# Kernel tuning notes

Measured on AMD Instinct MI355X. Metric: run time of the kernel, lower is better.

## Reference

```python
import jax, jax.numpy as jnp
import numpy as np

BN_EPS = 1e-5

def setup_inputs() -> dict:
    key = jax.random.key(0)
    k1, k2, k3 = jax.random.split(key, 3)
    B, N, C, K, O = 4, 16384, 64, 16, 64
    x = jax.random.normal(k1, (B, N, C), dtype=jnp.float32)
    idx = jax.random.randint(k2, (B, N, K), 0, N, dtype=jnp.int32)
    weight = jax.random.normal(k3, (O, 2 * C), dtype=jnp.float32) * 0.05
    gamma = jnp.ones((O,), dtype=jnp.float32)
    beta = jnp.zeros((O,), dtype=jnp.float32)
    return {"x": x, "idx": idx, "weight": weight, "gamma": gamma, "beta": beta}

def reference(x, idx, weight, gamma, beta):
    # x: [B,N,C], idx: [B,N,k] kNN indices into N
    B, N, C = x.shape
    k = idx.shape[2]
    # irregular gather: neighbor features [B,N,k,C]
    batch_ix = jnp.arange(B)[:, None, None]
    neighbor = x[batch_ix, idx]                     # [B,N,k,C]
    center = x[:, :, None, :]                       # [B,N,1,C]
    diff = neighbor - center                        # [B,N,k,C]
    edge = jnp.concatenate([jnp.broadcast_to(center, (B, N, k, C)), diff], axis=-1)  # [B,N,k,2C]
    # 1x1 conv == per-edge linear transform: [B,N,k,O]
    h = jnp.einsum('bnkc,oc->bnko', edge, weight)
    # BatchNorm2d in training mode: stats over (B,N,k) per output channel
    mean = jnp.mean(h, axis=(0, 1, 2))
    var = jnp.var(h, axis=(0, 1, 2))
    h = (h - mean) * jax.lax.rsqrt(var + BN_EPS) * gamma + beta
    h = jax.nn.relu(h)
    # max-pool over k neighbors -> [B,N,O]
    out = jnp.max(h, axis=2)
    return out
```

## Files before the change

kernel.cpp:

```cpp
#include <hip/hip_runtime.h>
#include <math.h>

#define BN_EPS 1e-5f

constexpr int B_ = 4, N_ = 16384, C_ = 64, K_ = 16, O_ = 64;
constexpr int ROWS = B_ * N_;
constexpr int ROWS_PER_BLK = 64;
constexpr int NBLK_AB = ROWS / ROWS_PER_BLK;

__global__ __launch_bounds__(256) void pass_a(const float* __restrict__ x,
                                              const float* __restrict__ w,
                                              float* __restrict__ y1,
                                              float* __restrict__ y2) {
    __shared__ float w1m[64 * 65];
    __shared__ float w2s[64 * 65];
    __shared__ float xs[64 * 64];
    const int tid = threadIdx.x;

    for (int i = tid; i < 64 * 64; i += 256) {
        int o = i >> 6, c = i & 63;
        float a = w[o * 128 + c];
        float b = w[o * 128 + 64 + c];
        w1m[c * 65 + o] = a - b;
        w2s[c * 65 + o] = b;
    }
    const long base = (long)blockIdx.x * ROWS_PER_BLK;
    const float* xsrc = x + base * 64;
    for (int i = tid; i < 64 * 64; i += 256) xs[i] = xsrc[i];
    __syncthreads();

    const int o  = tid & 63;
    const int rr = tid >> 6;
    for (int chunk = 0; chunk < 4; ++chunk) {
        const int r0 = chunk * 16 + rr * 4;
        float a1[4] = {0.f, 0.f, 0.f, 0.f};
        float a2[4] = {0.f, 0.f, 0.f, 0.f};
        for (int c4 = 0; c4 < 16; ++c4) {
            float4 xv[4];
#pragma unroll
            for (int j = 0; j < 4; ++j)
                xv[j] = *(const float4*)&xs[(r0 + j) * 64 + c4 * 4];
#pragma unroll
            for (int cc = 0; cc < 4; ++cc) {
                const int c = c4 * 4 + cc;
                const float wv1 = w1m[c * 65 + o];
                const float wv2 = w2s[c * 65 + o];
                const float xj0 = (&xv[0].x)[cc], xj1 = (&xv[1].x)[cc];
                const float xj2 = (&xv[2].x)[cc], xj3 = (&xv[3].x)[cc];
                a1[0] = fmaf(xj0, wv1, a1[0]); a2[0] = fmaf(xj0, wv2, a2[0]);
                a1[1] = fmaf(xj1, wv1, a1[1]); a2[1] = fmaf(xj1, wv2, a2[1]);
                a1[2] = fmaf(xj2, wv1, a1[2]); a2[2] = fmaf(xj2, wv2, a2[2]);
                a1[3] = fmaf(xj3, wv1, a1[3]); a2[3] = fmaf(xj3, wv2, a2[3]);
            }
        }
#pragma unroll
        for (int j = 0; j < 4; ++j) {
            y1[(base + r0 + j) * 64 + o] = a1[j];
            y2[(base + r0 + j) * 64 + o] = a2[j];
        }
    }
}

__global__ __launch_bounds__(256) void pass_b(const float* __restrict__ y1,
                                              const float* __restrict__ y2,
                                              const int* __restrict__ idx,
                                              const float* __restrict__ gamma,
                                              float* __restrict__ exth,
                                              float* __restrict__ partial) {
    __shared__ int sidx[ROWS_PER_BLK * K_];
    __shared__ float reds[4][64];
    __shared__ float redq[4][64];
    const int tid = threadIdx.x;
    const int blk = blockIdx.x;
    const int xcd = blk & 7;
    const int bt = xcd >> 1;
    const int slot = ((blk >> 3) << 1) | (xcd & 1);
    const long base = (long)bt * N_ + (long)slot * ROWS_PER_BLK;

    ((int4*)sidx)[tid] = ((const int4*)(idx + base * K_))[tid];

    const int lane = tid & 63;
    const int wv   = tid >> 6;
    const int ksub = lane >> 4;
    const int c4   = lane & 15;
    const float* y2b = y2 + (long)bt * N_ * 64;

    const float4 gm = ((const float4*)gamma)[c4];
    const float4 sgn = make_float4(gm.x >= 0.f ? 1.f : -1.f,
                                   gm.y >= 0.f ? 1.f : -1.f,
                                   gm.z >= 0.f ? 1.f : -1.f,
                                   gm.w >= 0.f ? 1.f : -1.f);
    __syncthreads();

    float4 psum = make_float4(0.f, 0.f, 0.f, 0.f);
    float4 psq  = make_float4(0.f, 0.f, 0.f, 0.f);

    for (int rl = wv; rl < ROWS_PER_BLK; rl += 4) {
        const long row = base + rl;
        const float4 y1v = ((const float4*)(y1 + row * 64))[c4];
        float4 e = make_float4(-3.402823466e+38f, -3.402823466e+38f,
                               -3.402823466e+38f, -3.402823466e+38f);
#pragma unroll
        for (int kk = 0; kk < 4; ++kk) {
            const int m = sidx[rl * K_ + kk * 4 + ksub];
            const float4 v = *(const float4*)(y2b + (long)m * 64 + c4 * 4);
            const float hx = y1v.x + v.x, hy = y1v.y + v.y;
            const float hz = y1v.z + v.z, hw = y1v.w + v.w;
            e.x = fmaxf(e.x, sgn.x * hx); e.y = fmaxf(e.y, sgn.y * hy);
            e.z = fmaxf(e.z, sgn.z * hz); e.w = fmaxf(e.w, sgn.w * hw);
            psum.x += hx; psum.y += hy; psum.z += hz; psum.w += hw;
            psq.x = fmaf(hx, hx, psq.x); psq.y = fmaf(hy, hy, psq.y);
            psq.z = fmaf(hz, hz, psq.z); psq.w = fmaf(hw, hw, psq.w);
        }
#pragma unroll
        for (int d = 16; d <= 32; d <<= 1) {
            e.x = fmaxf(e.x, __shfl_xor(e.x, d));
            e.y = fmaxf(e.y, __shfl_xor(e.y, d));
            e.z = fmaxf(e.z, __shfl_xor(e.z, d));
            e.w = fmaxf(e.w, __shfl_xor(e.w, d));
        }
        if (ksub == 0) {
            float4 r = make_float4(sgn.x * e.x, sgn.y * e.y,
                                   sgn.z * e.z, sgn.w * e.w);
            *(float4*)(exth + row * 64 + c4 * 4) = r;
        }
    }
#pragma unroll
    for (int d = 16; d <= 32; d <<= 1) {
        psum.x += __shfl_xor(psum.x, d); psum.y += __shfl_xor(psum.y, d);
        psum.z += __shfl_xor(psum.z, d); psum.w += __shfl_xor(psum.w, d);
        psq.x  += __shfl_xor(psq.x, d);  psq.y  += __shfl_xor(psq.y, d);
        psq.z  += __shfl_xor(psq.z, d);  psq.w  += __shfl_xor(psq.w, d);
    }
    if (ksub == 0) {
        *(float4*)&reds[wv][c4 * 4] = psum;
        *(float4*)&redq[wv][c4 * 4] = psq;
    }
    __syncthreads();
    if (tid < 64) {
        const float s = reds[0][tid] + reds[1][tid] + reds[2][tid] + reds[3][tid];
        const float q = redq[0][tid] + redq[1][tid] + redq[2][tid] + redq[3][tid];
        partial[blk * 128 + tid] = s;
        partial[blk * 128 + 64 + tid] = q;
    }
}

__global__ __launch_bounds__(256) void pass_c(const float* __restrict__ partial,
                                              const float* __restrict__ gamma,
                                              const float* __restrict__ beta,
                                              float* __restrict__ ss) {
    __shared__ double rs[256];
    __shared__ double rq[256];
    const int o = blockIdx.x;
    const int tid = threadIdx.x;
    double as = 0.0, aq = 0.0;
    for (int i = tid; i < NBLK_AB; i += 256) {
        as += (double)partial[i * 128 + o];
        aq += (double)partial[i * 128 + 64 + o];
    }
    rs[tid] = as;
    rq[tid] = aq;
    __syncthreads();
    for (int s = 128; s > 0; s >>= 1) {
        if (tid < s) { rs[tid] += rs[tid + s]; rq[tid] += rq[tid + s]; }
        __syncthreads();
    }
    if (tid == 0) {
        const double cnt = (double)B_ * N_ * K_;
        double mean = rs[0] / cnt;
        double var = rq[0] / cnt - mean * mean;
        float scale = gamma[o] * (float)(1.0 / sqrt(var + (double)BN_EPS));
        float shift = beta[o] - (float)mean * scale;
        ss[o] = scale;
        ss[64 + o] = shift;
    }
}

__global__ __launch_bounds__(256) void pass_d(const float* __restrict__ exth,
                                              const float* __restrict__ ss,
                                              float* __restrict__ out) {
    __shared__ float sscale[64], sshift[64];
    const int tid = threadIdx.x;
    if (tid < 64) { sscale[tid] = ss[tid]; sshift[tid] = ss[64 + tid]; }
    __syncthreads();
    const float4* ep = (const float4*)exth;
    float4* op = (float4*)out;
    const long total4 = (long)ROWS * 64 / 4;
    for (long i = (long)blockIdx.x * 256 + tid; i < total4;
         i += (long)gridDim.x * 256) {
        const int c0 = ((int)i * 4) & 63;
        float4 e = ep[i];
        float4 r;
        r.x = fmaxf(fmaf(sscale[c0],     e.x, sshift[c0]),     0.f);
        r.y = fmaxf(fmaf(sscale[c0 + 1], e.y, sshift[c0 + 1]), 0.f);
        r.z = fmaxf(fmaf(sscale[c0 + 2], e.z, sshift[c0 + 2]), 0.f);
        r.w = fmaxf(fmaf(sscale[c0 + 3], e.w, sshift[c0 + 3]), 0.f);
        op[i] = r;
    }
}

extern "C" void kernel_launch(void* const* d_in, const int* in_sizes, int n_in,
                              void* d_out, int out_size, void* d_ws, size_t ws_size,
                              hipStream_t stream) {
    const float* x     = (const float*)d_in[0];
    const int*   idx   = (const int*)d_in[1];
    const float* w     = (const float*)d_in[2];
    const float* gamma = (const float*)d_in[3];
    const float* beta  = (const float*)d_in[4];
    float* out = (float*)d_out;

    float* ws = (float*)d_ws;
    float* y1      = ws;
    float* y2      = y1 + (long)ROWS * 64;
    float* exth    = y2 + (long)ROWS * 64;
    float* partial = exth + (long)ROWS * 64;
    float* ss      = partial + (long)NBLK_AB * 128;

    pass_a<<<NBLK_AB, 256, 0, stream>>>(x, w, y1, y2);
    pass_b<<<NBLK_AB, 256, 0, stream>>>(y1, y2, idx, gamma, exth, partial);
    pass_c<<<64, 256, 0, stream>>>(partial, gamma, beta, ss);
    pass_d<<<2048, 256, 0, stream>>>(exth, ss, out);
}
```

Measured before the change: 123.7 us.

## Register-tile pass_a GEMM, batch gathers in pass_b, add nontemporal loads/stores

```diff
diff --git a/kernel.cpp b/kernel.cpp
--- a/kernel.cpp
+++ b/kernel.cpp
@@ -8,56 +8,95 @@
 constexpr int ROWS_PER_BLK = 64;
 constexpr int NBLK_AB = ROWS / ROWS_PER_BLK;
 
+typedef float  vf4 __attribute__((ext_vector_type(4)));
+typedef int    vi4 __attribute__((ext_vector_type(4)));
+
+__device__ __forceinline__ float4 nt_load4(const float* p) {
+    vf4 v = __builtin_nontemporal_load((const vf4*)p);
+    return make_float4(v.x, v.y, v.z, v.w);
+}
+__device__ __forceinline__ void nt_store4(float* p, float4 v) {
+    vf4 t; t.x = v.x; t.y = v.y; t.z = v.z; t.w = v.w;
+    __builtin_nontemporal_store(t, (vf4*)p);
+}
+
 __global__ __launch_bounds__(256) void pass_a(const float* __restrict__ x,
                                               const float* __restrict__ w,
                                               float* __restrict__ y1,
                                               float* __restrict__ y2) {
-    __shared__ float w1m[64 * 65];
-    __shared__ float w2s[64 * 65];
-    __shared__ float xs[64 * 64];
-    const int tid = threadIdx.x;
-
-    for (int i = tid; i < 64 * 64; i += 256) {
-        int o = i >> 6, c = i & 63;
-        float a = w[o * 128 + c];
-        float b = w[o * 128 + 64 + c];
-        w1m[c * 65 + o] = a - b;
-        w2s[c * 65 + o] = b;
-    }
-    const long base = (long)blockIdx.x * ROWS_PER_BLK;
+    __shared__ __align__(16) float xs[64 * 68];
+    __shared__ __align__(16) float w1m[64 * 64];
+    __shared__ __align__(16) float w2s[64 * 64];
+    const int tid = threadIdx.x;
+
+    const int blk = blockIdx.x;
+    const int xcd = blk & 7;
+    const int bt = xcd >> 1;
+    const int slot = ((blk >> 3) << 1) | (xcd & 1);
+    const long base = (long)bt * N_ + (long)slot * ROWS_PER_BLK;
+
+    for (int i = tid; i < 64 * 16; i += 256) {
+        const int o = i & 63;
+        const int c4 = i >> 6;
+        const float4 wa = *(const float4*)&w[o * 128 + c4 * 4];
+        const float4 wb = *(const float4*)&w[o * 128 + 64 + c4 * 4];
+        w1m[(c4 * 4 + 0) * 64 + o] = wa.x - wb.x;
+        w1m[(c4 * 4 + 1) * 64 + o] = wa.y - wb.y;
+        w1m[(c4 * 4 + 2) * 64 + o] = wa.z - wb.z;
+        w1m[(c4 * 4 + 3) * 64 + o] = wa.w - wb.w;
+        w2s[(c4 * 4 + 0) * 64 + o] = wb.x;
+        w2s[(c4 * 4 + 1) * 64 + o] = wb.y;
+        w2s[(c4 * 4 + 2) * 64 + o] = wb.z;
+        w2s[(c4 * 4 + 3) * 64 + o] = wb.w;
+    }
+
     const float* xsrc = x + base * 64;
-    for (int i = tid; i < 64 * 64; i += 256) xs[i] = xsrc[i];
-    __syncthreads();
-
-    const int o  = tid & 63;
-    const int rr = tid >> 6;
-    for (int chunk = 0; chunk < 4; ++chunk) {
-        const int r0 = chunk * 16 + rr * 4;
-        float a1[4] = {0.f, 0.f, 0.f, 0.f};
-        float a2[4] = {0.f, 0.f, 0.f, 0.f};
-        for (int c4 = 0; c4 < 16; ++c4) {
-            float4 xv[4];
-#pragma unroll
-            for (int j = 0; j < 4; ++j)
-                xv[j] = *(const float4*)&xs[(r0 + j) * 64 + c4 * 4];
-#pragma unroll
-            for (int cc = 0; cc < 4; ++cc) {
-                const int c = c4 * 4 + cc;
-                const float wv1 = w1m[c * 65 + o];
-                const float wv2 = w2s[c * 65 + o];
-                const float xj0 = (&xv[0].x)[cc], xj1 = (&xv[1].x)[cc];
-                const float xj2 = (&xv[2].x)[cc], xj3 = (&xv[3].x)[cc];
-                a1[0] = fmaf(xj0, wv1, a1[0]); a2[0] = fmaf(xj0, wv2, a2[0]);
-                a1[1] = fmaf(xj1, wv1, a1[1]); a2[1] = fmaf(xj1, wv2, a2[1]);
-                a1[2] = fmaf(xj2, wv1, a1[2]); a2[2] = fmaf(xj2, wv2, a2[2]);
-                a1[3] = fmaf(xj3, wv1, a1[3]); a2[3] = fmaf(xj3, wv2, a2[3]);
-            }
-        }
-#pragma unroll
-        for (int j = 0; j < 4; ++j) {
-            y1[(base + r0 + j) * 64 + o] = a1[j];
-            y2[(base + r0 + j) * 64 + o] = a2[j];
-        }
+    for (int i = tid; i < 64 * 16; i += 256) {
+        const int row = i >> 4;
+        const int c4 = i & 15;
+        const float4 v = nt_load4(xsrc + i * 4);
+        xs[(c4 * 4 + 0) * 68 + row] = v.x;
+        xs[(c4 * 4 + 1) * 68 + row] = v.y;
+        xs[(c4 * 4 + 2) * 68 + row] = v.z;
+        xs[(c4 * 4 + 3) * 68 + row] = v.w;
+    }
+    __syncthreads();
+
+    const int o0 = (tid & 15) * 4;
+    const int r0 = (tid >> 4) * 4;
+    float a1[4][4] = {{0.f}};
+    float a2[4][4] = {{0.f}};
+
+#pragma unroll 4
+    for (int c = 0; c < 64; ++c) {
+        const float4 xv = *(const float4*)&xs[c * 68 + r0];
+        const float4 w1v = *(const float4*)&w1m[c * 64 + o0];
+        const float4 w2v = *(const float4*)&w2s[c * 64 + o0];
+        const float xr0 = xv.x, xr1 = xv.y, xr2 = xv.z, xr3 = xv.w;
+        a1[0][0] = fmaf(xr0, w1v.x, a1[0][0]); a1[0][1] = fmaf(xr0, w1v.y, a1[0][1]);
+        a1[0][2] = fmaf(xr0, w1v.z, a1[0][2]); a1[0][3] = fmaf(xr0, w1v.w, a1[0][3]);
+        a2[0][0] = fmaf(xr0, w2v.x, a2[0][0]); a2[0][1] = fmaf(xr0, w2v.y, a2[0][1]);
+        a2[0][2] = fmaf(xr0, w2v.z, a2[0][2]); a2[0][3] = fmaf(xr0, w2v.w, a2[0][3]);
+        a1[1][0] = fmaf(xr1, w1v.x, a1[1][0]); a1[1][1] = fmaf(xr1, w1v.y, a1[1][1]);
+        a1[1][2] = fmaf(xr1, w1v.z, a1[1][2]); a1[1][3] = fmaf(xr1, w1v.w, a1[1][3]);
+        a2[1][0] = fmaf(xr1, w2v.x, a2[1][0]); a2[1][1] = fmaf(xr1, w2v.y, a2[1][1]);
+        a2[1][2] = fmaf(xr1, w2v.z, a2[1][2]); a2[1][3] = fmaf(xr1, w2v.w, a2[1][3]);
+        a1[2][0] = fmaf(xr2, w1v.x, a1[2][0]); a1[2][1] = fmaf(xr2, w1v.y, a1[2][1]);
+        a1[2][2] = fmaf(xr2, w1v.z, a1[2][2]); a1[2][3] = fmaf(xr2, w1v.w, a1[2][3]);
+        a2[2][0] = fmaf(xr2, w2v.x, a2[2][0]); a2[2][1] = fmaf(xr2, w2v.y, a2[2][1]);
+        a2[2][2] = fmaf(xr2, w2v.z, a2[2][2]); a2[2][3] = fmaf(xr2, w2v.w, a2[2][3]);
+        a1[3][0] = fmaf(xr3, w1v.x, a1[3][0]); a1[3][1] = fmaf(xr3, w1v.y, a1[3][1]);
+        a1[3][2] = fmaf(xr3, w1v.z, a1[3][2]); a1[3][3] = fmaf(xr3, w1v.w, a1[3][3]);
+        a2[3][0] = fmaf(xr3, w2v.x, a2[3][0]); a2[3][1] = fmaf(xr3, w2v.y, a2[3][1]);
+        a2[3][2] = fmaf(xr3, w2v.z, a2[3][2]); a2[3][3] = fmaf(xr3, w2v.w, a2[3][3]);
+    }
+
+#pragma unroll
+    for (int r = 0; r < 4; ++r) {
+        *(float4*)&y1[(base + r0 + r) * 64 + o0] =
+            make_float4(a1[r][0], a1[r][1], a1[r][2], a1[r][3]);
+        *(float4*)&y2[(base + r0 + r) * 64 + o0] =
+            make_float4(a2[r][0], a2[r][1], a2[r][2], a2[r][3]);
     }
 }
 
@@ -77,7 +116,11 @@
     const int slot = ((blk >> 3) << 1) | (xcd & 1);
     const long base = (long)bt * N_ + (long)slot * ROWS_PER_BLK;
 
-    ((int4*)sidx)[tid] = ((const int4*)(idx + base * K_))[tid];
+    {
+        vi4 iv = __builtin_nontemporal_load(
+            (const vi4*)(idx + base * K_) + tid);
+        ((vi4*)sidx)[tid] = iv;
+    }
 
     const int lane = tid & 63;
     const int wv   = tid >> 6;
@@ -95,34 +138,64 @@
     float4 psum = make_float4(0.f, 0.f, 0.f, 0.f);
     float4 psq  = make_float4(0.f, 0.f, 0.f, 0.f);
 
-    for (int rl = wv; rl < ROWS_PER_BLK; rl += 4) {
-        const long row = base + rl;
-        const float4 y1v = ((const float4*)(y1 + row * 64))[c4];
-        float4 e = make_float4(-3.402823466e+38f, -3.402823466e+38f,
-                               -3.402823466e+38f, -3.402823466e+38f);
+    for (int rl = wv; rl < ROWS_PER_BLK; rl += 8) {
+        const long rowA = base + rl;
+        const long rowB = base + rl + 4;
+        float4 vA[4], vB[4];
 #pragma unroll
         for (int kk = 0; kk < 4; ++kk) {
             const int m = sidx[rl * K_ + kk * 4 + ksub];
-            const float4 v = *(const float4*)(y2b + (long)m * 64 + c4 * 4);
-            const float hx = y1v.x + v.x, hy = y1v.y + v.y;
-            const float hz = y1v.z + v.z, hw = y1v.w + v.w;
-            e.x = fmaxf(e.x, sgn.x * hx); e.y = fmaxf(e.y, sgn.y * hy);
-            e.z = fmaxf(e.z, sgn.z * hz); e.w = fmaxf(e.w, sgn.w * hw);
+            vA[kk] = *(const float4*)(y2b + (long)m * 64 + c4 * 4);
+        }
+#pragma unroll
+        for (int kk = 0; kk < 4; ++kk) {
+            const int m = sidx[(rl + 4) * K_ + kk * 4 + ksub];
+            vB[kk] = *(const float4*)(y2b + (long)m * 64 + c4 * 4);
+        }
+        const float4 y1A = nt_load4(y1 + rowA * 64 + c4 * 4);
+        const float4 y1B = nt_load4(y1 + rowB * 64 + c4 * 4);
+
+        float4 eA = make_float4(-3.402823466e+38f, -3.402823466e+38f,
+                                -3.402823466e+38f, -3.402823466e+38f);
+        float4 eB = eA;
+#pragma unroll
+        for (int kk = 0; kk < 4; ++kk) {
+            const float hx = y1A.x + vA[kk].x, hy = y1A.y + vA[kk].y;
+            const float hz = y1A.z + vA[kk].z, hw = y1A.w + vA[kk].w;
+            eA.x = fmaxf(eA.x, sgn.x * hx); eA.y = fmaxf(eA.y, sgn.y * hy);
+            eA.z = fmaxf(eA.z, sgn.z * hz); eA.w = fmaxf(eA.w, sgn.w * hw);
             psum.x += hx; psum.y += hy; psum.z += hz; psum.w += hw;
             psq.x = fmaf(hx, hx, psq.x); psq.y = fmaf(hy, hy, psq.y);
             psq.z = fmaf(hz, hz, psq.z); psq.w = fmaf(hw, hw, psq.w);
         }
 #pragma unroll
+        for (int kk = 0; kk < 4; ++kk) {
+            const float hx = y1B.x + vB[kk].x, hy = y1B.y + vB[kk].y;
+            const float hz = y1B.z + vB[kk].z, hw = y1B.w + vB[kk].w;
+            eB.x = fmaxf(eB.x, sgn.x * hx); eB.y = fmaxf(eB.y, sgn.y * hy);
+            eB.z = fmaxf(eB.z, sgn.z * hz); eB.w = fmaxf(eB.w, sgn.w * hw);
+            psum.x += hx; psum.y += hy; psum.z += hz; psum.w += hw;
+            psq.x = fmaf(hx, hx, psq.x); psq.y = fmaf(hy, hy, psq.y);
+            psq.z = fmaf(hz, hz, psq.z); psq.w = fmaf(hw, hw, psq.w);
+        }
+#pragma unroll
         for (int d = 16; d <= 32; d <<= 1) {
-            e.x = fmaxf(e.x, __shfl_xor(e.x, d));
-            e.y = fmaxf(e.y, __shfl_xor(e.y, d));
-            e.z = fmaxf(e.z, __shfl_xor(e.z, d));
-            e.w = fmaxf(e.w, __shfl_xor(e.w, d));
+            eA.x = fmaxf(eA.x, __shfl_xor(eA.x, d));
+            eA.y = fmaxf(eA.y, __shfl_xor(eA.y, d));
+            eA.z = fmaxf(eA.z, __shfl_xor(eA.z, d));
+            eA.w = fmaxf(eA.w, __shfl_xor(eA.w, d));
+            eB.x = fmaxf(eB.x, __shfl_xor(eB.x, d));
+            eB.y = fmaxf(eB.y, __shfl_xor(eB.y, d));
+            eB.z = fmaxf(eB.z, __shfl_xor(eB.z, d));
+            eB.w = fmaxf(eB.w, __shfl_xor(eB.w, d));
         }
         if (ksub == 0) {
-            float4 r = make_float4(sgn.x * e.x, sgn.y * e.y,
-                                   sgn.z * e.z, sgn.w * e.w);
-            *(float4*)(exth + row * 64 + c4 * 4) = r;
+            float4 rA = make_float4(sgn.x * eA.x, sgn.y * eA.y,
+                                    sgn.z * eA.z, sgn.w * eA.w);
+            float4 rB = make_float4(sgn.x * eB.x, sgn.y * eB.y,
+                                    sgn.z * eB.z, sgn.w * eB.w);
+            nt_store4(exth + rowA * 64 + c4 * 4, rA);
+            nt_store4(exth + rowB * 64 + c4 * 4, rB);
         }
     }
 #pragma unroll
@@ -183,19 +256,17 @@
     const int tid = threadIdx.x;
     if (tid < 64) { sscale[tid] = ss[tid]; sshift[tid] = ss[64 + tid]; }
     __syncthreads();
-    const float4* ep = (const float4*)exth;
-    float4* op = (float4*)out;
     const long total4 = (long)ROWS * 64 / 4;
     for (long i = (long)blockIdx.x * 256 + tid; i < total4;
          i += (long)gridDim.x * 256) {
         const int c0 = ((int)i * 4) & 63;
-        float4 e = ep[i];
+        float4 e = nt_load4(exth + i * 4);
         float4 r;
         r.x = fmaxf(fmaf(sscale[c0],     e.x, sshift[c0]),     0.f);
         r.y = fmaxf(fmaf(sscale[c0 + 1], e.y, sshift[c0 + 1]), 0.f);
         r.z = fmaxf(fmaf(sscale[c0 + 2], e.z, sshift[c0 + 2]), 0.f);
         r.w = fmaxf(fmaf(sscale[c0 + 3], e.w, sshift[c0 + 3]), 0.f);
-        op[i] = r;
+        nt_store4((float*)out + i * 4, r);
     }
 }
 
```

After: 125.3 us. About the same (+1.2%).
